# Kernel optimization log

Measured on AMD Instinct MI355X. Metric: run time of the kernel, lower is better.

The kernel has to match this reference:

```python
import jax, jax.numpy as jnp
import numpy as np

B, T, C, H = 8, 2048, 1024, 64
SCALE = H ** -0.5


def setup_inputs() -> dict:
    key = jax.random.key(0)
    kx, kq, kk, kv = jax.random.split(key, 4)
    x = jax.random.normal(kx, (B, T, C), dtype=jnp.float32)
    w_q = jax.random.normal(kq, (C, H), dtype=jnp.float32) * (C ** -0.5)
    w_k = jax.random.normal(kk, (C, H), dtype=jnp.float32) * (C ** -0.5)
    w_v = jax.random.normal(kv, (C, H), dtype=jnp.float32) * (C ** -0.5)
    return {"x": x, "w_q": w_q, "w_k": w_k, "w_v": w_v}


def reference(x, w_q, w_k, w_v):
    # Projections: [B,T,C] @ [C,H] -> [B,T,H]
    q = jnp.einsum('btc,ch->bth', x, w_q)
    k = jnp.einsum('btc,ch->bth', x, w_k)
    v = jnp.einsum('btc,ch->bth', x, w_v)
    # Scaled scores [B,T,T], causal mask, softmax (dropout p=0 -> identity)
    wei = jnp.einsum('bqh,bkh->bqk', q, k) * SCALE
    tq = x.shape[1]
    causal = jnp.tril(jnp.ones((tq, tq), dtype=bool))
    wei = jnp.where(causal[None, :, :], wei, -jnp.inf)
    wei = jax.nn.softmax(wei, axis=-1)
    out = jnp.einsum('bqk,bkh->bqh', wei, v)
    return out
```

## Files before the change

### kernel.cpp

```cpp
#include <hip/hip_runtime.h>
#include <hip/hip_bf16.h>
#include <cstdint>

#define TB 8
#define TT 2048
#define TC 1024
#define TH 64

typedef __bf16 bf16;
typedef __bf16 bf16x2 __attribute__((ext_vector_type(2)));
typedef __bf16 bf16x4 __attribute__((ext_vector_type(4)));
typedef __bf16 bf16x8 __attribute__((ext_vector_type(8)));
typedef float  f32x4  __attribute__((ext_vector_type(4)));

constexpr float QSCALE = 0.125f * 1.44269504088896340736f;

__device__ __forceinline__ void gll16(const void* g, void* l) {
    __builtin_amdgcn_global_load_lds((const __attribute__((address_space(1))) unsigned int*)g,
                                     (__attribute__((address_space(3))) unsigned int*)l, 16, 0, 0);
}

#define WAIT_VM0()   __builtin_amdgcn_s_waitcnt(0x0F70)
#define WAIT_LGKM0() __builtin_amdgcn_s_waitcnt(0xC07F)

__global__ void prep_wT(const float* __restrict__ wq, const float* __restrict__ wk,
                        const float* __restrict__ wv, bf16* __restrict__ wT) {
    int idx = blockIdx.x * blockDim.x + threadIdx.x;
    if (idx >= 3 * TH * TC) return;
    int wsel = idx / (TH * TC);
    int rem  = idx % (TH * TC);
    int c = rem / TH;
    int h = rem % TH;
    const float* w = (wsel == 0) ? wq : (wsel == 1) ? wk : wv;
    wT[(size_t)wsel * TH * TC + (size_t)h * TC + c] = (bf16)w[(size_t)c * TH + h];
}

__launch_bounds__(256)
__global__ void proj(const float* __restrict__ x, const bf16* __restrict__ wT,
                     bf16* __restrict__ Q, bf16* __restrict__ K, bf16* __restrict__ VT) {
    __shared__ __align__(16) char lds[49152];
    const int tid  = threadIdx.x;
    const int wv   = tid >> 6;
    const int lane = tid & 63;
    const int quad = lane >> 4, l16 = lane & 15;
    const int wsel = blockIdx.x % 3;
    const int m0   = (blockIdx.x / 3) * 64;

    const float* xb = x  + (size_t)m0 * TC;
    const bf16*  wb = wT + (size_t)wsel * (TH * TC);

    f32x4 acc[4];
#pragma unroll
    for (int g = 0; g < 4; g++) acc[g] = f32x4{0.f, 0.f, 0.f, 0.f};

    const int lr16 = lane >> 4, lc16 = lane & 15;
    const int lr8  = lane >> 3, lc8  = lane & 7;

#define STAGE(kc, bb)                                                          \
    {                                                                          \
        _Pragma("unroll")                                                      \
        for (int i = 0; i < 4; i++) {                                          \
            int base_row = wv * 16 + i * 4;                                    \
            int row = base_row + lr16;                                         \
            int c = lc16 ^ (row & 15);                                         \
            gll16(xb + (size_t)row * TC + (kc) * 64 + c * 4,                   \
                  lds + (bb) * 16384 + base_row * 256);                        \
        }                                                                      \
        _Pragma("unroll")                                                      \
        for (int i = 0; i < 2; i++) {                                          \
            int base_col = i * 32 + wv * 8;                                    \
            int col = base_col + lr8;                                          \
            int c = lc8 ^ (col & 7);                                           \
            gll16(wb + (size_t)col * TC + (kc) * 64 + c * 8,                   \
                  lds + 32768 + (bb) * 8192 + base_col * 128);                 \
        }                                                                      \
    }

    STAGE(0, 0);
    for (int kc = 0; kc < 16; kc++) {
        const int cur = kc & 1;
        __syncthreads();
        if (kc + 1 < 16) STAGE(kc + 1, cur ^ 1);
        const char* Xb = lds + cur * 16384;
        const char* Wb = lds + 32768 + cur * 8192;
        const int row = wv * 16 + l16;
#pragma unroll
        for (int s = 0; s < 2; s++) {
            int c1 = (s * 8 + 2 * quad) ^ l16;
            int c2 = (s * 8 + 2 * quad + 1) ^ l16;
            f32x4 a0 = *(const f32x4*)(Xb + row * 256 + c1 * 16);
            f32x4 a1 = *(const f32x4*)(Xb + row * 256 + c2 * 16);
            bf16x8 af;
            af[0] = (bf16)a0[0]; af[1] = (bf16)a0[1]; af[2] = (bf16)a0[2]; af[3] = (bf16)a0[3];
            af[4] = (bf16)a1[0]; af[5] = (bf16)a1[1]; af[6] = (bf16)a1[2]; af[7] = (bf16)a1[3];
#pragma unroll
            for (int g = 0; g < 4; g++) {
                int col = g * 16 + l16;
                int c = (s * 4 + quad) ^ (col & 7);
                bf16x8 bq = *(const bf16x8*)(Wb + col * 128 + c * 16);
                acc[g] = __builtin_amdgcn_mfma_f32_16x16x32_bf16(af, bq, acc[g], 0, 0, 0);
            }
        }
    }

    const int mrow = m0 + wv * 16 + quad * 4;
    if (wsel == 0) {
#pragma unroll
        for (int g = 0; g < 4; g++) {
            int col = g * 16 + l16;
#pragma unroll
            for (int r = 0; r < 4; r++)
                Q[(size_t)(mrow + r) * TH + col] = (bf16)(acc[g][r] * QSCALE);
        }
    } else if (wsel == 1) {
#pragma unroll
        for (int g = 0; g < 4; g++) {
            int col = g * 16 + l16;
#pragma unroll
            for (int r = 0; r < 4; r++)
                K[(size_t)(mrow + r) * TH + col] = (bf16)acc[g][r];
        }
    } else {
        const int b = m0 >> 11;
        const int t = mrow & 2047;
#pragma unroll
        for (int g = 0; g < 4; g++) {
            int col = g * 16 + l16;
            bf16x4 o;
#pragma unroll
            for (int r = 0; r < 4; r++) o[r] = (bf16)acc[g][r];
            *(bf16x4*)(VT + ((size_t)b * TH + col) * TT + t) = o;
        }
    }
}
#undef STAGE

__device__ __forceinline__ float packbf(float a, float b) {
    union { bf16x2 h; float f; } u;
    u.h[0] = (bf16)a; u.h[1] = (bf16)b;
    return u.f;
}

__launch_bounds__(256, 2)
__global__ void attn(const bf16* __restrict__ Q, const bf16* __restrict__ K,
                     const bf16* __restrict__ VT, float* __restrict__ out) {
    __shared__ __align__(16) char lds[65536];

    const int tid  = threadIdx.x;
    const int wv   = tid >> 6;
    const int lane = tid & 63;
    const int quad = lane >> 4, l16 = lane & 15;
    const int b  = blockIdx.x & 7;
    const int qc = 63 - (blockIdx.x >> 3);
    const int q0 = qc * 32;
    const int ktd = qc >> 1;

    char* Kst = lds + wv * 16384;
    char* Vst = Kst + 8192;

    const bf16* Qb = Q  + (size_t)b * TT * TH;
    const bf16* Kb = K  + (size_t)b * TT * TH;
    const bf16* Vb = VT + (size_t)b * TH * TT;

    bf16x8 bq[2][2];
#pragma unroll
    for (int qg = 0; qg < 2; qg++)
#pragma unroll
        for (int kh = 0; kh < 2; kh++)
            bq[qg][kh] = *(const bf16x8*)(Qb + (size_t)(q0 + qg * 16 + l16) * TH + kh * 32 + quad * 8);

    f32x4 accO[2][4];
#pragma unroll
    for (int qg = 0; qg < 2; qg++)
#pragma unroll
        for (int g = 0; g < 4; g++) accO[qg][g] = f32x4{0.f, 0.f, 0.f, 0.f};
    float mI[2] = {-1e30f, -1e30f}, lI[2] = {0.f, 0.f};

    const int r8 = lane >> 3, c8 = lane & 7;
    const int src1 = (quad & 1) * 32 + l16;
    const int src2 = src1 + 16;

#define STAGEKV(kt_)                                                            \
    {                                                                           \
        const int k0_ = (kt_) * 64;                                             \
        _Pragma("unroll")                                                       \
        for (int i = 0; i < 8; i++) {                                           \
            int t = i * 8 + r8;                                                 \
            gll16((const char*)Kb + (size_t)(k0_ + t) * 128 + ((c8 ^ (t & 7)) << 4), \
                  Kst + i * 1024);                                              \
        }                                                                       \
        _Pragma("unroll")                                                       \
        for (int i = 0; i < 8; i++) {                                           \
            int h = i * 8 + r8;                                                 \
            gll16((const char*)Vb + ((size_t)h * TT + k0_) * 2 + ((c8 ^ (h & 7)) << 4), \
                  Vst + i * 1024);                                              \
        }                                                                       \
    }

    if (wv <= ktd) {
        STAGEKV(wv);
        for (int kt = wv; kt <= ktd; kt += 4) {
            WAIT_VM0();
            bf16x8 ka[4][2], bv[4][2];
#pragma unroll
            for (int g = 0; g < 4; g++) {
                int t = g * 16 + l16;
                const char* kr = Kst + t * 128;
                ka[g][0] = *(const bf16x8*)(kr + ((quad ^ (t & 7)) << 4));
                ka[g][1] = *(const bf16x8*)(kr + (((4 + quad) ^ (t & 7)) << 4));
                const char* vr = Vst + t * 128;
                bv[g][0] = *(const bf16x8*)(vr + ((quad ^ (t & 7)) << 4));
                bv[g][1] = *(const bf16x8*)(vr + (((4 + quad) ^ (t & 7)) << 4));
            }
            WAIT_LGKM0();
            if (kt + 4 <= ktd) STAGEKV(kt + 4);

            f32x4 s[2][4];
#pragma unroll
            for (int g = 0; g < 4; g++)
#pragma unroll
                for (int qg = 0; qg < 2; qg++) {
                    f32x4 t0 = f32x4{0.f, 0.f, 0.f, 0.f};
                    t0 = __builtin_amdgcn_mfma_f32_16x16x32_bf16(ka[g][0], bq[qg][0], t0, 0, 0, 0);
                    t0 = __builtin_amdgcn_mfma_f32_16x16x32_bf16(ka[g][1], bq[qg][1], t0, 0, 0, 0);
                    s[qg][g] = t0;
                }

            if (kt == ktd) {
#pragma unroll
                for (int qg = 0; qg < 2; qg++) {
                    const int qrel = ((qc & 1) << 5) + qg * 16 + l16;
#pragma unroll
                    for (int g = 0; g < 4; g++)
#pragma unroll
                        for (int r = 0; r < 4; r++)
                            if (g * 16 + quad * 4 + r > qrel) s[qg][g][r] = -3.0e38f;
                }
            }

            float alpha[2];
#pragma unroll
            for (int qg = 0; qg < 2; qg++) {
                float m = s[qg][0][0];
#pragma unroll
                for (int g = 0; g < 4; g++)
#pragma unroll
                    for (int r = 0; r < 4; r++) m = fmaxf(m, s[qg][g][r]);
                m = fmaxf(m, __shfl_xor(m, 16));
                m = fmaxf(m, __shfl_xor(m, 32));
                float mnew = fmaxf(mI[qg], m);
                float a = __builtin_amdgcn_exp2f(mI[qg] - mnew);
                mI[qg] = mnew;
                float rs = 0.f;
#pragma unroll
                for (int g = 0; g < 4; g++)
#pragma unroll
                    for (int r = 0; r < 4; r++) {
                        float p = __builtin_amdgcn_exp2f(s[qg][g][r] - mnew);
                        s[qg][g][r] = p;
                        rs += p;
                    }
                rs += __shfl_xor(rs, 16);
                rs += __shfl_xor(rs, 32);
                lI[qg] = lI[qg] * a + rs;
                alpha[qg] = a;
            }
#pragma unroll
            for (int qg = 0; qg < 2; qg++) {
                float ar[4];
#pragma unroll
                for (int r = 0; r < 4; r++) ar[r] = __shfl(alpha[qg], quad * 4 + r);
#pragma unroll
                for (int g = 0; g < 4; g++)
#pragma unroll
                    for (int r = 0; r < 4; r++) accO[qg][g][r] *= ar[r];
            }

            float pk[2][4][2];
#pragma unroll
            for (int qg = 0; qg < 2; qg++)
#pragma unroll
                for (int g = 0; g < 4; g++) {
                    pk[qg][g][0] = packbf(s[qg][g][0], s[qg][g][1]);
                    pk[qg][g][1] = packbf(s[qg][g][2], s[qg][g][3]);
                }

#pragma unroll
            for (int c = 0; c < 2; c++) {
#pragma unroll
                for (int qg = 0; qg < 2; qg++) {
                    float A0p0 = __shfl(pk[qg][c * 2][0], src1);
                    float A0p1 = __shfl(pk[qg][c * 2][1], src1);
                    float B0p0 = __shfl(pk[qg][c * 2][0], src2);
                    float B0p1 = __shfl(pk[qg][c * 2][1], src2);
                    float A1p0 = __shfl(pk[qg][c * 2 + 1][0], src1);
                    float A1p1 = __shfl(pk[qg][c * 2 + 1][1], src1);
                    float B1p0 = __shfl(pk[qg][c * 2 + 1][0], src2);
                    float B1p1 = __shfl(pk[qg][c * 2 + 1][1], src2);
                    bool lo = quad < 2;
                    union { float4 f; bf16x8 v; } u;
                    u.f = make_float4(lo ? A0p0 : A1p0, lo ? A0p1 : A1p1,
                                      lo ? B0p0 : B1p0, lo ? B0p1 : B1p1);
#pragma unroll
                    for (int g = 0; g < 4; g++)
                        accO[qg][g] = __builtin_amdgcn_mfma_f32_16x16x32_bf16(u.v, bv[g][c], accO[qg][g], 0, 0, 0);
                }
            }
        }
    }
#undef STAGEKV

    __syncthreads();
    float* Omg = (float*)lds;
    float* Mmg = (float*)(lds + 34816);
    float* Lmg = (float*)(lds + 35328);
#pragma unroll
    for (int qg = 0; qg < 2; qg++)
#pragma unroll
        for (int g = 0; g < 4; g++)
#pragma unroll
            for (int r = 0; r < 4; r++)
                Omg[(size_t)(wv * 32 + qg * 16 + quad * 4 + r) * 68 + g * 16 + l16] = accO[qg][g][r];
    if (quad == 0) {
#pragma unroll
        for (int qg = 0; qg < 2; qg++) {
            Mmg[wv * 32 + qg * 16 + l16] = mI[qg];
            Lmg[wv * 32 + qg * 16 + l16] = lI[qg];
        }
    }
    __syncthreads();

#pragma unroll
    for (int p = 0; p < 2; p++) {
        const int idx = p * 256 + tid;
        const int q = idx >> 4;
        const int hs = (idx & 15) * 4;
        float gm = Mmg[q];
#pragma unroll
        for (int w = 1; w < 4; w++) gm = fmaxf(gm, Mmg[w * 32 + q]);
        float denom = 0.f, o0 = 0.f, o1 = 0.f, o2 = 0.f, o3 = 0.f;
#pragma unroll
        for (int w = 0; w < 4; w++) {
            float sc = __builtin_amdgcn_exp2f(Mmg[w * 32 + q] - gm);
            denom += Lmg[w * 32 + q] * sc;
            const float* op = Omg + (size_t)(w * 32 + q) * 68 + hs;
            o0 += op[0] * sc; o1 += op[1] * sc; o2 += op[2] * sc; o3 += op[3] * sc;
        }
        float inv = 1.f / denom;
        *(float4*)(out + ((size_t)b * TT + q0 + q) * TH + hs) =
            make_float4(o0 * inv, o1 * inv, o2 * inv, o3 * inv);
    }
}

extern "C" void kernel_launch(void* const* d_in, const int* in_sizes, int n_in,
                              void* d_out, int out_size, void* d_ws, size_t ws_size,
                              hipStream_t stream) {
    const float* x  = (const float*)d_in[0];
    const float* wq = (const float*)d_in[1];
    const float* wk = (const float*)d_in[2];
    const float* wv = (const float*)d_in[3];

    char* ws = (char*)d_ws;
    bf16*  wT = (bf16*)(ws);
    bf16*  Q  = (bf16*)(ws + 393216);
    bf16*  K  = (bf16*)(ws + 2490368);
    bf16*  VT = (bf16*)(ws + 4587520);
    float* out = (float*)d_out;

    hipLaunchKernelGGL(prep_wT, dim3(768), dim3(256), 0, stream, wq, wk, wv, wT);
    hipLaunchKernelGGL(proj, dim3(768), dim3(256), 0, stream, x, wT, Q, K, VT);
    hipLaunchKernelGGL(attn, dim3(TB * 64), dim3(256), 0, stream, Q, K, VT, out);
}
```

Before: 139.1 us.

## Halve attention KV tile to 32 keys and double-buffer KV staging

```diff
diff --git a/kernel.cpp b/kernel.cpp
--- a/kernel.cpp
+++ b/kernel.cpp
@@ -21,6 +21,7 @@
 }
 
 #define WAIT_VM0()   __builtin_amdgcn_s_waitcnt(0x0F70)
+#define WAIT_VM8()   __builtin_amdgcn_s_waitcnt(0x0F78)
 #define WAIT_LGKM0() __builtin_amdgcn_s_waitcnt(0xC07F)
 
 __global__ void prep_wT(const float* __restrict__ wq, const float* __restrict__ wk,
@@ -153,7 +154,6 @@
     const int b  = blockIdx.x & 7;
     const int qc = 63 - (blockIdx.x >> 3);
     const int q0 = qc * 32;
-    const int ktd = qc >> 1;
 
     char* Kst = lds + wv * 16384;
     char* Vst = Kst + 8192;
@@ -177,47 +177,58 @@
     float mI[2] = {-1e30f, -1e30f}, lI[2] = {0.f, 0.f};
 
     const int r8 = lane >> 3, c8 = lane & 7;
+    const int r4 = lane >> 2, c4 = lane & 3;
     const int src1 = (quad & 1) * 32 + l16;
     const int src2 = src1 + 16;
 
-#define STAGEKV(kt_)                                                            \
+#define STAGEKV(kt_, bb_)                                                       \
     {                                                                           \
-        const int k0_ = (kt_) * 64;                                             \
+        const int k0_ = (kt_) * 32;                                             \
         _Pragma("unroll")                                                       \
-        for (int i = 0; i < 8; i++) {                                           \
+        for (int i = 0; i < 4; i++) {                                           \
             int t = i * 8 + r8;                                                 \
-            gll16((const char*)Kb + (size_t)(k0_ + t) * 128 + ((c8 ^ (t & 7)) << 4), \
-                  Kst + i * 1024);                                              \
+            gll16(Kb + (size_t)(k0_ + t) * 64 + ((c8 ^ r8) * 8),                \
+                  Kst + (bb_) * 4096 + i * 1024);                               \
         }                                                                       \
         _Pragma("unroll")                                                       \
-        for (int i = 0; i < 8; i++) {                                           \
-            int h = i * 8 + r8;                                                 \
-            gll16((const char*)Vb + ((size_t)h * TT + k0_) * 2 + ((c8 ^ (h & 7)) << 4), \
-                  Vst + i * 1024);                                              \
+        for (int i = 0; i < 4; i++) {                                           \
+            int h = i * 16 + r4;                                                \
+            gll16(Vb + (size_t)h * TT + k0_ + ((c4 ^ quad) * 8),                \
+                  Vst + (bb_) * 4096 + i * 1024);                               \
         }                                                                       \
     }
 
-    if (wv <= ktd) {
-        STAGEKV(wv);
-        for (int kt = wv; kt <= ktd; kt += 4) {
-            WAIT_VM0();
-            bf16x8 ka[4][2], bv[4][2];
+    if (wv <= qc) {
+        const int kt1 = (wv + 4 <= qc) ? wv + 4 : qc;
+        STAGEKV(wv, 0);
+        STAGEKV(kt1, 1);
+        int nit = 0;
+        for (int kt = wv; kt <= qc; kt += 4, nit++) {
+            const int bb = nit & 1;
+            WAIT_VM8();
+
+            bf16x8 ka[2][2], bv[4];
+#pragma unroll
+            for (int g = 0; g < 2; g++) {
+                int t = g * 16 + l16;
+                const char* kr = Kst + bb * 4096 + t * 128;
+                ka[g][0] = *(const bf16x8*)(kr + (((quad) ^ (t & 7)) << 4));
+                ka[g][1] = *(const bf16x8*)(kr + (((4 + quad) ^ (t & 7)) << 4));
+            }
 #pragma unroll
             for (int g = 0; g < 4; g++) {
-                int t = g * 16 + l16;
-                const char* kr = Kst + t * 128;
-                ka[g][0] = *(const bf16x8*)(kr + ((quad ^ (t & 7)) << 4));
-                ka[g][1] = *(const bf16x8*)(kr + (((4 + quad) ^ (t & 7)) << 4));
-                const char* vr = Vst + t * 128;
-                bv[g][0] = *(const bf16x8*)(vr + ((quad ^ (t & 7)) << 4));
-                bv[g][1] = *(const bf16x8*)(vr + (((4 + quad) ^ (t & 7)) << 4));
+                int h = g * 16 + l16;
+                bv[g] = *(const bf16x8*)(Vst + bb * 4096 + h * 64 + ((quad ^ (l16 >> 2)) << 4));
             }
             WAIT_LGKM0();
-            if (kt + 4 <= ktd) STAGEKV(kt + 4);
-
-            f32x4 s[2][4];
-#pragma unroll
-            for (int g = 0; g < 4; g++)
+            {
+                int ktn = kt + 8; if (ktn > qc) ktn = qc;
+                STAGEKV(ktn, bb);
+            }
+
+            f32x4 s[2][2];
+#pragma unroll
+            for (int g = 0; g < 2; g++)
 #pragma unroll
                 for (int qg = 0; qg < 2; qg++) {
                     f32x4 t0 = f32x4{0.f, 0.f, 0.f, 0.f};
@@ -226,15 +237,15 @@
                     s[qg][g] = t0;
                 }
 
-            if (kt == ktd) {
+            if (kt == qc) {
 #pragma unroll
                 for (int qg = 0; qg < 2; qg++) {
-                    const int qrel = ((qc & 1) << 5) + qg * 16 + l16;
-#pragma unroll
-                    for (int g = 0; g < 4; g++)
+                    const int ql = qg * 16 + l16;
+#pragma unroll
+                    for (int g = 0; g < 2; g++)
 #pragma unroll
                         for (int r = 0; r < 4; r++)
-                            if (g * 16 + quad * 4 + r > qrel) s[qg][g][r] = -3.0e38f;
+                            if (g * 16 + quad * 4 + r > ql) s[qg][g][r] = -3.0e38f;
                 }
             }
 
@@ -243,7 +254,7 @@
             for (int qg = 0; qg < 2; qg++) {
                 float m = s[qg][0][0];
 #pragma unroll
-                for (int g = 0; g < 4; g++)
+                for (int g = 0; g < 2; g++)
 #pragma unroll
                     for (int r = 0; r < 4; r++) m = fmaxf(m, s[qg][g][r]);
                 m = fmaxf(m, __shfl_xor(m, 16));
@@ -253,7 +264,7 @@
                 mI[qg] = mnew;
                 float rs = 0.f;
 #pragma unroll
-                for (int g = 0; g < 4; g++)
+                for (int g = 0; g < 2; g++)
 #pragma unroll
                     for (int r = 0; r < 4; r++) {
                         float p = __builtin_amdgcn_exp2f(s[qg][g][r] - mnew);
@@ -276,40 +287,29 @@
                     for (int r = 0; r < 4; r++) accO[qg][g][r] *= ar[r];
             }
 
-            float pk[2][4][2];
-#pragma unroll
-            for (int qg = 0; qg < 2; qg++)
-#pragma unroll
-                for (int g = 0; g < 4; g++) {
-                    pk[qg][g][0] = packbf(s[qg][g][0], s[qg][g][1]);
-                    pk[qg][g][1] = packbf(s[qg][g][2], s[qg][g][3]);
-                }
-
-#pragma unroll
-            for (int c = 0; c < 2; c++) {
-#pragma unroll
-                for (int qg = 0; qg < 2; qg++) {
-                    float A0p0 = __shfl(pk[qg][c * 2][0], src1);
-                    float A0p1 = __shfl(pk[qg][c * 2][1], src1);
-                    float B0p0 = __shfl(pk[qg][c * 2][0], src2);
-                    float B0p1 = __shfl(pk[qg][c * 2][1], src2);
-                    float A1p0 = __shfl(pk[qg][c * 2 + 1][0], src1);
-                    float A1p1 = __shfl(pk[qg][c * 2 + 1][1], src1);
-                    float B1p0 = __shfl(pk[qg][c * 2 + 1][0], src2);
-                    float B1p1 = __shfl(pk[qg][c * 2 + 1][1], src2);
-                    bool lo = quad < 2;
-                    union { float4 f; bf16x8 v; } u;
-                    u.f = make_float4(lo ? A0p0 : A1p0, lo ? A0p1 : A1p1,
-                                      lo ? B0p0 : B1p0, lo ? B0p1 : B1p1);
-#pragma unroll
-                    for (int g = 0; g < 4; g++)
-                        accO[qg][g] = __builtin_amdgcn_mfma_f32_16x16x32_bf16(u.v, bv[g][c], accO[qg][g], 0, 0, 0);
-                }
+#pragma unroll
+            for (int qg = 0; qg < 2; qg++) {
+                float p00 = packbf(s[qg][0][0], s[qg][0][1]);
+                float p01 = packbf(s[qg][0][2], s[qg][0][3]);
+                float p10 = packbf(s[qg][1][0], s[qg][1][1]);
+                float p11 = packbf(s[qg][1][2], s[qg][1][3]);
+                float A0p0 = __shfl(p00, src1), A0p1 = __shfl(p01, src1);
+                float B0p0 = __shfl(p00, src2), B0p1 = __shfl(p01, src2);
+                float A1p0 = __shfl(p10, src1), A1p1 = __shfl(p11, src1);
+                float B1p0 = __shfl(p10, src2), B1p1 = __shfl(p11, src2);
+                bool lo = quad < 2;
+                union { float4 f; bf16x8 v; } u;
+                u.f = make_float4(lo ? A0p0 : A1p0, lo ? A0p1 : A1p1,
+                                  lo ? B0p0 : B1p0, lo ? B0p1 : B1p1);
+#pragma unroll
+                for (int g = 0; g < 4; g++)
+                    accO[qg][g] = __builtin_amdgcn_mfma_f32_16x16x32_bf16(u.v, bv[g], accO[qg][g], 0, 0, 0);
             }
         }
     }
 #undef STAGEKV
 
+    WAIT_VM0();
     __syncthreads();
     float* Omg = (float*)lds;
     float* Mmg = (float*)(lds + 34816);
```

Result: slower. 141.9 us (+2.0%).
